# Kernel tuning notes

Hardware: AMD Instinct MI355X
Metric: run time of the kernel (lower is better)

The kernel has to match this reference:

```python
import jax, jax.numpy as jnp
import numpy as np

B, N, DIM = 4, 2048, 128
K = 32            # num_nearest_neighbors
FF = 4            # fourier_features
M_DIM = 16
EDGE_IN = FF * 2 + DIM * 2 + 1  # 265


def setup_inputs() -> dict:
    key = jax.random.key(0)
    ks = jax.random.split(key, 16)
    std = 0.001  # init_eps normal init for Linear weights
    p = {
        "feats": jax.random.normal(ks[0], (B, N, DIM), jnp.float32),
        "coors": jax.random.normal(ks[1], (B, N, 3), jnp.float32),
        # edge_mlp: Linear(265, 530) -> SiLU -> Linear(530, 16) -> SiLU
        "eW1": jax.random.normal(ks[2], (EDGE_IN, EDGE_IN * 2), jnp.float32) * std,
        "eb1": jax.random.normal(ks[3], (EDGE_IN * 2,), jnp.float32) * std,
        "eW2": jax.random.normal(ks[4], (EDGE_IN * 2, M_DIM), jnp.float32) * std,
        "eb2": jax.random.normal(ks[5], (M_DIM,), jnp.float32) * std,
        # coors_mlp: Linear(16, 64) -> SiLU -> Linear(64, 1)
        "cW1": jax.random.normal(ks[6], (M_DIM, M_DIM * 4), jnp.float32) * std,
        "cb1": jax.random.normal(ks[7], (M_DIM * 4,), jnp.float32) * std,
        "cW2": jax.random.normal(ks[8], (M_DIM * 4, 1), jnp.float32) * std,
        "cb2": jax.random.normal(ks[9], (1,), jnp.float32) * std,
        # node_mlp: Linear(144, 256) -> SiLU -> Linear(256, 128)
        "nW1": jax.random.normal(ks[10], (DIM + M_DIM, DIM * 2), jnp.float32) * std,
        "nb1": jax.random.normal(ks[11], (DIM * 2,), jnp.float32) * std,
        "nW2": jax.random.normal(ks[12], (DIM * 2, DIM), jnp.float32) * std,
        "nb2": jax.random.normal(ks[13], (DIM,), jnp.float32) * std,
    }
    return p


def _egnn_fwd(feats, coors, eW1, eb1, eW2, eb2, cW1, cb1, cW2, cb2, nW1, nb1, nW2, nb2):
    # all-pairs squared distances: [b, n, n]
    rel_coors_full = coors[:, :, None, :] - coors[:, None, :, :]
    rel_dist = jnp.sum(rel_coors_full * rel_coors_full, axis=-1)

    # top-k nearest (smallest distance) -> indices [b, n, k]
    _, idx = jax.lax.top_k(-rel_dist, K)

    # gather neighbor coords / feats per batch: [b, n, k, *]
    coors_j = jax.vmap(lambda x, i: x[i])(coors, idx)
    feats_j = jax.vmap(lambda x, i: x[i])(feats, idx)
    rel_coors = coors[:, :, None, :] - coors_j                     # b n k 3
    d = jnp.take_along_axis(rel_dist, idx, axis=2)[..., None]       # b n k 1

    # fourier encode distances: [b, n, k, 2*FF + 1]
    scales = 2.0 ** jnp.arange(FF, dtype=feats.dtype)               # [FF]
    xs = d[..., None] / scales                                      # b n k 1 FF
    enc = jnp.concatenate([jnp.sin(xs), jnp.cos(xs), d[..., None]], axis=-1)
    enc = enc[..., 0, :]                                            # b n k (2FF+1)

    feats_i = jnp.broadcast_to(feats[:, :, None, :], feats_j.shape)
    edge_input = jnp.concatenate([feats_i, feats_j, enc], axis=-1)  # b n k 265

    # edge MLP -> messages m_ij [b, n, k, m_dim]
    h = jax.nn.silu(edge_input @ eW1 + eb1)
    m_ij = jax.nn.silu(h @ eW2 + eb2)

    # coors MLP -> per-edge coordinate weights [b, n, k]
    cw = (jax.nn.silu(m_ij @ cW1 + cb1) @ cW2 + cb2)[..., 0]
    coors_out = jnp.einsum('bij,bijc->bic', cw, rel_coors) + coors

    # node update: sum-pool messages, concat with feats, MLP + residual
    m_i = jnp.sum(m_ij, axis=-2)                                    # b n m_dim
    node_in = jnp.concatenate([feats, m_i], axis=-1)
    node_out = jax.nn.silu(node_in @ nW1 + nb1) @ nW2 + nb2 + feats
    return node_out, coors_out


def reference(feats, coors, eW1, eb1, eW2, eb2, cW1, cb1, cW2, cb2, nW1, nb1, nW2, nb2):
    return _egnn_fwd(feats, coors, eW1, eb1, eW2, eb2, cW1, cb1, cW2, cb2, nW1, nb1, nW2, nb2)
```

## Files before the change

kernel.cpp:

```cpp
#include <hip/hip_runtime.h>
#include <hip/hip_bf16.h>
#include <math.h>

#define Bb 4
#define Nn 2048
#define DIMd 128
#define Kk 32
#define H1 530
#define PW2 530
#define MD 16
#define NDH 256
#define NDI 144
#define TOPK_BLKS (Bb*Nn/4)
#define PMAT_BLKS (Bb*Nn/32)

typedef float f32x2 __attribute__((ext_vector_type(2)));
typedef float f32x4 __attribute__((ext_vector_type(4)));
typedef short s16x8 __attribute__((ext_vector_type(8)));

__device__ __forceinline__ unsigned short f2bf(float f){
    union { float f; unsigned u; } v; v.f = f;
    unsigned r = v.u + 0x7FFFu + ((v.u >> 16) & 1u);
    return (unsigned short)(r >> 16);
}
__device__ __forceinline__ float silu_f(float x){
    float e = __builtin_amdgcn_exp2f(x * -1.442695041f);
    return x * __builtin_amdgcn_rcpf(1.0f + e);
}
__device__ __forceinline__ f32x2 silu2(f32x2 x){
    float e0 = __builtin_amdgcn_exp2f(x[0] * -1.442695041f);
    float e1 = __builtin_amdgcn_exp2f(x[1] * -1.442695041f);
    f32x2 r;
    r[0] = x[0] * __builtin_amdgcn_rcpf(1.0f + e0);
    r[1] = x[1] * __builtin_amdgcn_rcpf(1.0f + e1);
    return r;
}
__device__ __forceinline__ unsigned cvt_pk_bf16(float a, float b){
    unsigned r;
    asm("v_cvt_pk_bf16_f32 %0, %1, %2" : "=v"(r) : "v"(a), "v"(b));
    return r;
}

__global__ __launch_bounds__(256) void fragw_kernel(const float* __restrict__ eW1,
        const float* __restrict__ eW2,
        unsigned short* __restrict__ W1F, unsigned short* __restrict__ WPF,
        unsigned short* __restrict__ W2F2){
    int i0 = blockIdx.x * 256 + threadIdx.x;
    int stride = gridDim.x * 256;
    for (int i = i0; i < 34*5*512; i += stride){
        int j = i & 7, lane = (i >> 3) & 63, t = i >> 9;
        int ks = t % 5, nt = t / 5;
        int cg = nt*16 + (lane & 15);
        int k = ks*32 + ((lane >> 4) << 3) + j;
        float v = 0.f;
        if (cg < H1){
            if (k < 128) v = eW1[(size_t)(128+k)*H1 + cg];
            else if (k < 137) v = eW1[(size_t)(256+(k-128))*H1 + cg];
        }
        W1F[i] = f2bf(v);
    }
    for (int i = i0; i < 34*4*512; i += stride){
        int j = i & 7, lane = (i >> 3) & 63, t = i >> 9;
        int ks = t & 3, nt = t >> 2;
        int cg = nt*16 + (lane & 15);
        int k = ks*32 + ((lane >> 4) << 3) + j;
        float v = (cg < H1) ? eW1[(size_t)k*H1 + cg] : 0.f;
        WPF[i] = f2bf(v);
    }
    for (int i = i0; i < 34*512; i += stride){
        int j = i & 7, lane = (i >> 3) & 63, nt = i >> 9;
        int kl = ((lane >> 4) << 3) + j;
        int col = lane & 15;
        int row = nt*16 + kl;
        float v = (kl < 16 && row < H1) ? eW2[(size_t)row*MD + col] : 0.f;
        W2F2[i] = f2bf(v);
    }
}

__global__ __launch_bounds__(256) void prep_kernel(const float* __restrict__ coors,
        const float* __restrict__ feats,
        const unsigned short* __restrict__ WPF, const float* __restrict__ eb1,
        int* __restrict__ idx_ws, float* __restrict__ dv_ws, float* __restrict__ P){
    int bid = blockIdx.x;
    int tid = threadIdx.x;
    if (bid < TOPK_BLKS){
        int w = tid >> 6, lane = tid & 63;
        int node = bid * 4 + w;
        int b = node >> 11;
        const float* cbp = coors + (size_t)b * Nn * 3;
        float cx = coors[node*3+0], cy = coors[node*3+1], cz = coors[node*3+2];
        float d[32];
        #pragma unroll
        for (int t = 0; t < 32; t++){
            int j = t*64 + lane;
            float dx = cx - cbp[j*3+0], dy = cy - cbp[j*3+1], dz = cz - cbp[j*3+2];
            d[t] = dx*dx + dy*dy + dz*dz;
        }
        float md = d[0]; int mj = lane;
        #pragma unroll
        for (int t = 1; t < 32; t++){
            int jt = t*64 + lane;
            if (d[t] < md){ md = d[t]; mj = jt; }
        }
        for (int r = 0; r < Kk; r++){
            float bd = md; int bj = mj;
            #pragma unroll
            for (int off = 32; off; off >>= 1){
                float d2 = __shfl_xor(bd, off); int j2 = __shfl_xor(bj, off);
                if (d2 < bd || (d2 == bd && j2 < bj)){ bd = d2; bj = j2; }
            }
            if (lane == 0){
                idx_ws[node*Kk + r] = bj;
                dv_ws[node*Kk + r] = bd;
            }
            if (mj == bj){
                md = 3.4e38f; mj = 0x7fffffff;
                #pragma unroll
                for (int t = 0; t < 32; t++){
                    int jt = t*64 + lane;
                    if (jt == bj) d[t] = 3.4e38f;
                    if (d[t] < md){ md = d[t]; mj = jt; }
                }
            }
        }
    } else {
        int wid = tid >> 6, lane = tid & 63;
        int node0 = (bid - TOPK_BLKS) * 32;
        int kg = (lane >> 4) * 8;
        s16x8 af[2][4];
        #pragma unroll
        for (int m = 0; m < 2; m++){
            const float* fr = feats + (size_t)(node0 + m*16 + (lane & 15)) * DIMd;
            #pragma unroll
            for (int ks = 0; ks < 4; ks++){
                f32x4 lo = *(const f32x4*)(fr + ks*32 + kg);
                f32x4 hi = *(const f32x4*)(fr + ks*32 + kg + 4);
                union { s16x8 v; unsigned u[4]; } pk;
                pk.u[0] = cvt_pk_bf16(lo[0], lo[1]); pk.u[1] = cvt_pk_bf16(lo[2], lo[3]);
                pk.u[2] = cvt_pk_bf16(hi[0], hi[1]); pk.u[3] = cvt_pk_bf16(hi[2], hi[3]);
                af[m][ks] = pk.v;
            }
        }
        const s16x8* WPFv = (const s16x8*)WPF;
        for (int nt = wid; nt < 34; nt += 4){
            f32x4 acc0 = {0,0,0,0}, acc1 = {0,0,0,0};
            #pragma unroll
            for (int ks = 0; ks < 4; ks++){
                s16x8 bb = WPFv[(nt*4 + ks)*64 + lane];
                acc0 = __builtin_amdgcn_mfma_f32_16x16x32_bf16(af[0][ks], bb, acc0, 0, 0, 0);
                acc1 = __builtin_amdgcn_mfma_f32_16x16x32_bf16(af[1][ks], bb, acc1, 0, 0, 0);
            }
            int cg = nt*16 + (lane & 15);
            if (cg < H1){
                float b = eb1[cg];
                int r0 = (lane >> 4) * 4;
                #pragma unroll
                for (int r = 0; r < 4; r++){
                    P[(size_t)(node0 + r0 + r)*PW2 + cg]      = acc0[r] + b;
                    P[(size_t)(node0 + 16 + r0 + r)*PW2 + cg] = acc1[r] + b;
                }
            }
        }
    }
}

__global__ __launch_bounds__(256, 6) void edge_kernel(
        const float* __restrict__ feats, const float* __restrict__ eb2,
        const float* __restrict__ P, const unsigned short* __restrict__ W1F,
        const unsigned short* __restrict__ W2F2,
        const int* __restrict__ idx_ws, const float* __restrict__ dv_ws,
        float* __restrict__ m_ws){
    __shared__ float Pi_lds[544];
    __shared__ __align__(16) unsigned short aenc[Kk][32];
    __shared__ int js[Kk];
    __shared__ float m_red[4][Kk][MD+1];

    int node = blockIdx.x; int tid = threadIdx.x;
    int b = node >> 11;
    int wid = tid >> 6, lane = tid & 63;

    const float* Pn = P + (size_t)node*PW2;
    Pi_lds[tid]       = Pn[tid];
    { int c = tid + 256; Pi_lds[c] = (c < PW2) ? Pn[c] : 0.f; }
    if (tid < 32){ int c = 512 + tid; Pi_lds[c] = (c < PW2) ? Pn[c] : 0.f; }
    if (tid < Kk){
        int j = idx_ws[node*Kk + tid];
        float dv = dv_ws[node*Kk + tid];
        js[tid] = j;
        unsigned short e[9];
        e[0] = f2bf(sinf(dv));        e[1] = f2bf(sinf(dv*0.5f));
        e[2] = f2bf(sinf(dv*0.25f));  e[3] = f2bf(sinf(dv*0.125f));
        e[4] = f2bf(cosf(dv));        e[5] = f2bf(cosf(dv*0.5f));
        e[6] = f2bf(cosf(dv*0.25f));  e[7] = f2bf(cosf(dv*0.125f));
        e[8] = f2bf(dv);
        #pragma unroll
        for (int q = 0; q < 9; q++) aenc[tid][q] = e[q];
        #pragma unroll
        for (int q = 9; q < 32; q++) aenc[tid][q] = 0;
    }
    __syncthreads();

    int kg = (lane >> 4) * 8;
    int grp = lane >> 4, n16 = lane & 15;
    s16x8 af[2][5];
    #pragma unroll
    for (int m = 0; m < 2; m++){
        int row = m*16 + n16;
        int jgl = (b << 11) + js[row];
        const float* fr = feats + (size_t)jgl * DIMd;
        #pragma unroll
        for (int ks = 0; ks < 4; ks++){
            f32x4 lo = *(const f32x4*)(fr + ks*32 + kg);
            f32x4 hi = *(const f32x4*)(fr + ks*32 + kg + 4);
            union { s16x8 v; unsigned u[4]; } pk;
            pk.u[0] = cvt_pk_bf16(lo[0], lo[1]); pk.u[1] = cvt_pk_bf16(lo[2], lo[3]);
            pk.u[2] = cvt_pk_bf16(hi[0], hi[1]); pk.u[3] = cvt_pk_bf16(hi[2], hi[3]);
            af[m][ks] = pk.v;
        }
        af[m][4] = *(const s16x8*)(&aenc[row][kg]);
    }

    int addr1 = ((((2*grp)    ) << 4) | n16) << 2;
    int addr2 = ((((2*grp) + 1) << 4) | n16) << 2;

    const s16x8* W1Fv  = (const s16x8*)W1F;
    const s16x8* W2F2v = (const s16x8*)W2F2;
    f32x4 macc0 = {0,0,0,0}, macc1 = {0,0,0,0};
    for (int nt = wid; nt < 34; nt += 4){
        f32x4 acc0 = {0,0,0,0}, acc1 = {0,0,0,0};
        #pragma unroll
        for (int ks = 0; ks < 5; ks++){
            s16x8 aw = W1Fv[(nt*5 + ks)*64 + lane];
            acc0 = __builtin_amdgcn_mfma_f32_16x16x32_bf16(aw, af[0][ks], acc0, 0, 0, 0);
            acc1 = __builtin_amdgcn_mfma_f32_16x16x32_bf16(aw, af[1][ks], acc1, 0, 0, 0);
        }
        s16x8 w2a = W2F2v[nt*64 + lane];
        int cgb = nt*16 + grp*4;
        float x0[4], x1[4];
        #pragma unroll
        for (int r = 0; r < 4; r++){
            float pic = Pi_lds[cgb + r];
            x0[r] = silu_f(acc0[r] + pic);
            x1[r] = silu_f(acc1[r] + pic);
        }
        unsigned p00 = cvt_pk_bf16(x0[0], x0[1]), p01 = cvt_pk_bf16(x0[2], x0[3]);
        unsigned p10 = cvt_pk_bf16(x1[0], x1[1]), p11 = cvt_pk_bf16(x1[2], x1[3]);
        union { s16x8 v; int u[4]; } b0, b1;
        b0.u[0] = __builtin_amdgcn_ds_bpermute(addr1, (int)p00);
        b0.u[1] = __builtin_amdgcn_ds_bpermute(addr1, (int)p01);
        b0.u[2] = __builtin_amdgcn_ds_bpermute(addr2, (int)p00);
        b0.u[3] = __builtin_amdgcn_ds_bpermute(addr2, (int)p01);
        b1.u[0] = __builtin_amdgcn_ds_bpermute(addr1, (int)p10);
        b1.u[1] = __builtin_amdgcn_ds_bpermute(addr1, (int)p11);
        b1.u[2] = __builtin_amdgcn_ds_bpermute(addr2, (int)p10);
        b1.u[3] = __builtin_amdgcn_ds_bpermute(addr2, (int)p11);
        macc0 = __builtin_amdgcn_mfma_f32_16x16x32_bf16(w2a, b0.v, macc0, 0, 0, 0);
        macc1 = __builtin_amdgcn_mfma_f32_16x16x32_bf16(w2a, b1.v, macc1, 0, 0, 0);
    }
    #pragma unroll
    for (int r = 0; r < 4; r++){
        m_red[wid][n16][grp*4 + r]      = macc0[r];
        m_red[wid][16 + n16][grp*4 + r] = macc1[r];
    }
    __syncthreads();
    #pragma unroll
    for (int t = tid; t < Kk*MD; t += 256){
        int n = t >> 4, f = t & 15;
        float s = m_red[0][n][f] + m_red[1][n][f] + m_red[2][n][f] + m_red[3][n][f];
        m_ws[(size_t)node*(Kk*MD) + t] = silu_f(s + eb2[f]);
    }
}

__global__ __launch_bounds__(256) void finish_kernel(const float* __restrict__ feats,
        const float* __restrict__ coors,
        const float* __restrict__ m_ws, const int* __restrict__ idx_ws,
        const float* __restrict__ cW1, const float* __restrict__ cb1,
        const float* __restrict__ cW2, const float* __restrict__ cb2,
        const float* __restrict__ nW1, const float* __restrict__ nb1,
        const float* __restrict__ nW2, const float* __restrict__ nb2,
        float* __restrict__ out, float* __restrict__ coors_out){
    __shared__ float msh[8][Kk][MD+1];
    __shared__ float insT[NDI][12];
    __shared__ float hsdT[NDH][12];
    int tid = threadIdx.x;
    int node0 = blockIdx.x * 8;
    const float* mp = m_ws + (size_t)node0*(Kk*MD);
    for (int t = tid; t < 8*Kk*MD; t += 256)
        msh[t >> 9][(t >> 4) & 31][t & 15] = mp[t];
    for (int t = tid; t < 8*DIMd; t += 256)
        insT[t & 127][t >> 7] = feats[(size_t)node0*DIMd + t];
    int nl = tid >> 5, n = tid & 31;
    int node = node0 + nl;
    int b = node >> 11;
    int j = idx_ws[node*Kk + n];
    int jg = (b << 11) + j;
    float rx = coors[node*3+0] - coors[jg*3+0];
    float ry = coors[node*3+1] - coors[jg*3+1];
    float rz = coors[node*3+2] - coors[jg*3+2];
    __syncthreads();
    if (tid < 128){
        int m = tid >> 4, f = tid & 15;
        float s = 0.f;
        #pragma unroll
        for (int q = 0; q < Kk; q++) s += msh[m][q][f];
        insT[DIMd + f][m] = s;
    }
    float mv[MD];
    #pragma unroll
    for (int f = 0; f < MD; f++) mv[f] = msh[nl][n][f];
    float p = 0.f;
    #pragma unroll 4
    for (int ug = 0; ug < 16; ug++){
        f32x4 a4 = *(const f32x4*)(cb1 + ug*4);
        #pragma unroll
        for (int f = 0; f < MD; f++){
            f32x4 w4 = *(const f32x4*)(cW1 + f*64 + ug*4);
            a4 += (f32x4){mv[f],mv[f],mv[f],mv[f]} * w4;
        }
        f32x4 c4 = *(const f32x4*)(cW2 + ug*4);
        p += silu_f(a4[0])*c4[0] + silu_f(a4[1])*c4[1]
           + silu_f(a4[2])*c4[2] + silu_f(a4[3])*c4[3];
    }
    float cw = p + cb2[0];
    float vx = cw*rx, vy = cw*ry, vz = cw*rz;
    #pragma unroll
    for (int off = 1; off < 32; off <<= 1){
        vx += __shfl_xor(vx, off); vy += __shfl_xor(vy, off); vz += __shfl_xor(vz, off);
    }
    if (n == 0){
        coors_out[node*3+0] = vx + coors[node*3+0];
        coors_out[node*3+1] = vy + coors[node*3+1];
        coors_out[node*3+2] = vz + coors[node*3+2];
    }
    __syncthreads();
    float bias = nb1[tid];
    f32x2 acc[4];
    #pragma unroll
    for (int q = 0; q < 4; q++) acc[q] = (f32x2){bias, bias};
    for (int k = 0; k < NDI; k++){
        float wv = nW1[(size_t)k*NDH + tid];
        f32x2 w2 = {wv, wv};
        acc[0] += *(const f32x2*)&insT[k][0] * w2;
        acc[1] += *(const f32x2*)&insT[k][2] * w2;
        acc[2] += *(const f32x2*)&insT[k][4] * w2;
        acc[3] += *(const f32x2*)&insT[k][6] * w2;
    }
    #pragma unroll
    for (int q = 0; q < 4; q++) *(f32x2*)&hsdT[tid][2*q] = silu2(acc[q]);
    __syncthreads();
    int c = tid & 127, half = tid >> 7;
    float b2 = nb2[c];
    f32x2 a0 = {b2, b2}, a1 = {b2, b2};
    for (int k = 0; k < NDH; k++){
        float wv = nW2[(size_t)k*DIMd + c];
        f32x2 w2 = {wv, wv};
        a0 += *(const f32x2*)&hsdT[k][half*4]     * w2;
        a1 += *(const f32x2*)&hsdT[k][half*4 + 2] * w2;
    }
    #pragma unroll
    for (int q = 0; q < 4; q++){
        int m = half*4 + q;
        float v = (q < 2) ? a0[q & 1] : a1[q & 1];
        out[(size_t)(node0+m)*DIMd + c] = v + feats[(size_t)(node0+m)*DIMd + c];
    }
}

extern "C" void kernel_launch(void* const* d_in, const int* in_sizes, int n_in,
                              void* d_out, int out_size, void* d_ws, size_t ws_size,
                              hipStream_t stream){
    const float* feats = (const float*)d_in[0];
    const float* coors = (const float*)d_in[1];
    const float* eW1 = (const float*)d_in[2];
    const float* eb1 = (const float*)d_in[3];
    const float* eW2 = (const float*)d_in[4];
    const float* eb2 = (const float*)d_in[5];
    const float* cW1 = (const float*)d_in[6];
    const float* cb1 = (const float*)d_in[7];
    const float* cW2 = (const float*)d_in[8];
    const float* cb2 = (const float*)d_in[9];
    const float* nW1 = (const float*)d_in[10];
    const float* nb1 = (const float*)d_in[11];
    const float* nW2 = (const float*)d_in[12];
    const float* nb2 = (const float*)d_in[13];
    float* out = (float*)d_out;
    float* coors_out = out + (size_t)Bb*Nn*DIMd;

    char* ws = (char*)d_ws;
    size_t off = 0;
    int*   idx_ws = (int*)(ws + off);   off += (1u<<20);
    float* dv_ws  = (float*)(ws + off); off += (1u<<20);
    float* Pd     = (float*)(ws + off); off += 17367040u;
    float* m_ws   = (float*)(ws + off); off += 16777216u;
    unsigned short* W1F  = (unsigned short*)(ws + off); off += 174080u;
    unsigned short* WPF  = (unsigned short*)(ws + off); off += 139264u;
    unsigned short* W2F2 = (unsigned short*)(ws + off); off += 34816u;

    fragw_kernel<<<256, 256, 0, stream>>>(eW1, eW2, W1F, WPF, W2F2);
    prep_kernel<<<TOPK_BLKS + PMAT_BLKS, 256, 0, stream>>>(coors, feats, WPF, eb1,
                                                           idx_ws, dv_ws, Pd);
    edge_kernel<<<Bb*Nn, 256, 0, stream>>>(feats, eb2, Pd, W1F, W2F2,
                                           idx_ws, dv_ws, m_ws);
    finish_kernel<<<Bb*Nn/8, 256, 0, stream>>>(feats, coors, m_ws, idx_ws,
                                               cW1, cb1, cW2, cb2,
                                               nW1, nb1, nW2, nb2, out, coors_out);
}
```

Baseline: 297.3 us.

## Process two nodes per edge-kernel block to reuse W1 fragment loads

Each edge_kernel block now handles two nodes (64 edges) instead of one. Each W1/W2 weight fragment loaded from global memory feeds four MFMA column tiles instead of two, halving weight traffic per edge. The bpermute lane mapping is also changed. In exchange the kernel holds twice as many A fragments and accumulators in registers, so the launch bound drops from 6 to 4 blocks per SIMD. The grid is also halved, which could reduce latency hiding.

```diff
diff --git a/kernel.cpp b/kernel.cpp
--- a/kernel.cpp
+++ b/kernel.cpp
@@ -164,49 +164,53 @@
     }
 }
 
-__global__ __launch_bounds__(256, 6) void edge_kernel(
+__global__ __launch_bounds__(256, 4) void edge_kernel(
         const float* __restrict__ feats, const float* __restrict__ eb2,
         const float* __restrict__ P, const unsigned short* __restrict__ W1F,
         const unsigned short* __restrict__ W2F2,
         const int* __restrict__ idx_ws, const float* __restrict__ dv_ws,
         float* __restrict__ m_ws){
-    __shared__ float Pi_lds[544];
-    __shared__ __align__(16) unsigned short aenc[Kk][32];
-    __shared__ int js[Kk];
-    __shared__ float m_red[4][Kk][MD+1];
-
-    int node = blockIdx.x; int tid = threadIdx.x;
-    int b = node >> 11;
+    __shared__ float Pi_lds[2][544];
+    __shared__ __align__(16) unsigned short aenc[2][Kk][32];
+    __shared__ int js[2][Kk];
+    __shared__ float m_red[4][2][Kk][MD+1];
+
+    int node0 = blockIdx.x * 2;
+    int tid = threadIdx.x;
+    int b = node0 >> 11;
     int wid = tid >> 6, lane = tid & 63;
 
-    const float* Pn = P + (size_t)node*PW2;
-    Pi_lds[tid]       = Pn[tid];
-    { int c = tid + 256; Pi_lds[c] = (c < PW2) ? Pn[c] : 0.f; }
-    if (tid < 32){ int c = 512 + tid; Pi_lds[c] = (c < PW2) ? Pn[c] : 0.f; }
-    if (tid < Kk){
-        int j = idx_ws[node*Kk + tid];
-        float dv = dv_ws[node*Kk + tid];
-        js[tid] = j;
-        unsigned short e[9];
-        e[0] = f2bf(sinf(dv));        e[1] = f2bf(sinf(dv*0.5f));
-        e[2] = f2bf(sinf(dv*0.25f));  e[3] = f2bf(sinf(dv*0.125f));
-        e[4] = f2bf(cosf(dv));        e[5] = f2bf(cosf(dv*0.5f));
-        e[6] = f2bf(cosf(dv*0.25f));  e[7] = f2bf(cosf(dv*0.125f));
-        e[8] = f2bf(dv);
-        #pragma unroll
-        for (int q = 0; q < 9; q++) aenc[tid][q] = e[q];
-        #pragma unroll
-        for (int q = 9; q < 32; q++) aenc[tid][q] = 0;
+    for (int c = tid; c < 2*544; c += 256){
+        int nn = (c >= 544) ? 1 : 0;
+        int cc = c - nn*544;
+        Pi_lds[nn][cc] = (cc < PW2) ? P[(size_t)(node0+nn)*PW2 + cc] : 0.f;
+    }
+    if (tid < 64){
+        int nn = tid >> 5, e = tid & 31;
+        int j = idx_ws[(node0+nn)*Kk + e];
+        float dv = dv_ws[(node0+nn)*Kk + e];
+        js[nn][e] = j;
+        unsigned short ev[9];
+        ev[0] = f2bf(sinf(dv));        ev[1] = f2bf(sinf(dv*0.5f));
+        ev[2] = f2bf(sinf(dv*0.25f));  ev[3] = f2bf(sinf(dv*0.125f));
+        ev[4] = f2bf(cosf(dv));        ev[5] = f2bf(cosf(dv*0.5f));
+        ev[6] = f2bf(cosf(dv*0.25f));  ev[7] = f2bf(cosf(dv*0.125f));
+        ev[8] = f2bf(dv);
+        #pragma unroll
+        for (int q = 0; q < 9; q++) aenc[nn][e][q] = ev[q];
+        #pragma unroll
+        for (int q = 9; q < 32; q++) aenc[nn][e][q] = 0;
     }
     __syncthreads();
 
     int kg = (lane >> 4) * 8;
     int grp = lane >> 4, n16 = lane & 15;
-    s16x8 af[2][5];
-    #pragma unroll
-    for (int m = 0; m < 2; m++){
+    s16x8 af[4][5];
+    #pragma unroll
+    for (int s = 0; s < 4; s++){
+        int nn = s >> 1, m = s & 1;
         int row = m*16 + n16;
-        int jgl = (b << 11) + js[row];
+        int jgl = (b << 11) + js[nn][row];
         const float* fr = feats + (size_t)jgl * DIMd;
         #pragma unroll
         for (int ks = 0; ks < 4; ks++){
@@ -215,59 +219,94 @@
             union { s16x8 v; unsigned u[4]; } pk;
             pk.u[0] = cvt_pk_bf16(lo[0], lo[1]); pk.u[1] = cvt_pk_bf16(lo[2], lo[3]);
             pk.u[2] = cvt_pk_bf16(hi[0], hi[1]); pk.u[3] = cvt_pk_bf16(hi[2], hi[3]);
-            af[m][ks] = pk.v;
-        }
-        af[m][4] = *(const s16x8*)(&aenc[row][kg]);
-    }
-
-    int addr1 = ((((2*grp)    ) << 4) | n16) << 2;
-    int addr2 = ((((2*grp) + 1) << 4) | n16) << 2;
+            af[s][ks] = pk.v;
+        }
+        af[s][4] = *(const s16x8*)(&aenc[nn][row][kg]);
+    }
+
+    int s1 = ((grp & 1) << 1) | (grp >> 1);
+    int s2 = s1 ^ 1;
+    int addr1 = ((s1 << 4) | n16) << 2;
+    int addr2 = ((s2 << 4) | n16) << 2;
 
     const s16x8* W1Fv  = (const s16x8*)W1F;
     const s16x8* W2F2v = (const s16x8*)W2F2;
-    f32x4 macc0 = {0,0,0,0}, macc1 = {0,0,0,0};
+    f32x4 macc0 = {0,0,0,0}, macc1 = {0,0,0,0}, macc2 = {0,0,0,0}, macc3 = {0,0,0,0};
     for (int nt = wid; nt < 34; nt += 4){
-        f32x4 acc0 = {0,0,0,0}, acc1 = {0,0,0,0};
+        f32x4 acc0 = {0,0,0,0}, acc1 = {0,0,0,0}, acc2 = {0,0,0,0}, acc3 = {0,0,0,0};
         #pragma unroll
         for (int ks = 0; ks < 5; ks++){
             s16x8 aw = W1Fv[(nt*5 + ks)*64 + lane];
             acc0 = __builtin_amdgcn_mfma_f32_16x16x32_bf16(aw, af[0][ks], acc0, 0, 0, 0);
             acc1 = __builtin_amdgcn_mfma_f32_16x16x32_bf16(aw, af[1][ks], acc1, 0, 0, 0);
+            acc2 = __builtin_amdgcn_mfma_f32_16x16x32_bf16(aw, af[2][ks], acc2, 0, 0, 0);
+            acc3 = __builtin_amdgcn_mfma_f32_16x16x32_bf16(aw, af[3][ks], acc3, 0, 0, 0);
         }
         s16x8 w2a = W2F2v[nt*64 + lane];
         int cgb = nt*16 + grp*4;
-        float x0[4], x1[4];
-        #pragma unroll
-        for (int r = 0; r < 4; r++){
-            float pic = Pi_lds[cgb + r];
-            x0[r] = silu_f(acc0[r] + pic);
-            x1[r] = silu_f(acc1[r] + pic);
-        }
-        unsigned p00 = cvt_pk_bf16(x0[0], x0[1]), p01 = cvt_pk_bf16(x0[2], x0[3]);
-        unsigned p10 = cvt_pk_bf16(x1[0], x1[1]), p11 = cvt_pk_bf16(x1[2], x1[3]);
-        union { s16x8 v; int u[4]; } b0, b1;
-        b0.u[0] = __builtin_amdgcn_ds_bpermute(addr1, (int)p00);
-        b0.u[1] = __builtin_amdgcn_ds_bpermute(addr1, (int)p01);
-        b0.u[2] = __builtin_amdgcn_ds_bpermute(addr2, (int)p00);
-        b0.u[3] = __builtin_amdgcn_ds_bpermute(addr2, (int)p01);
-        b1.u[0] = __builtin_amdgcn_ds_bpermute(addr1, (int)p10);
-        b1.u[1] = __builtin_amdgcn_ds_bpermute(addr1, (int)p11);
-        b1.u[2] = __builtin_amdgcn_ds_bpermute(addr2, (int)p10);
-        b1.u[3] = __builtin_amdgcn_ds_bpermute(addr2, (int)p11);
-        macc0 = __builtin_amdgcn_mfma_f32_16x16x32_bf16(w2a, b0.v, macc0, 0, 0, 0);
-        macc1 = __builtin_amdgcn_mfma_f32_16x16x32_bf16(w2a, b1.v, macc1, 0, 0, 0);
+        {
+            float x[4];
+            #pragma unroll
+            for (int r = 0; r < 4; r++) x[r] = silu_f(acc0[r] + Pi_lds[0][cgb + r]);
+            unsigned p0 = cvt_pk_bf16(x[0], x[1]), p1 = cvt_pk_bf16(x[2], x[3]);
+            union { s16x8 v; int u[4]; } bb;
+            bb.u[0] = __builtin_amdgcn_ds_bpermute(addr1, (int)p0);
+            bb.u[1] = __builtin_amdgcn_ds_bpermute(addr1, (int)p1);
+            bb.u[2] = __builtin_amdgcn_ds_bpermute(addr2, (int)p0);
+            bb.u[3] = __builtin_amdgcn_ds_bpermute(addr2, (int)p1);
+            macc0 = __builtin_amdgcn_mfma_f32_16x16x32_bf16(w2a, bb.v, macc0, 0, 0, 0);
+        }
+        {
+            float x[4];
+            #pragma unroll
+            for (int r = 0; r < 4; r++) x[r] = silu_f(acc1[r] + Pi_lds[0][cgb + r]);
+            unsigned p0 = cvt_pk_bf16(x[0], x[1]), p1 = cvt_pk_bf16(x[2], x[3]);
+            union { s16x8 v; int u[4]; } bb;
+            bb.u[0] = __builtin_amdgcn_ds_bpermute(addr1, (int)p0);
+            bb.u[1] = __builtin_amdgcn_ds_bpermute(addr1, (int)p1);
+            bb.u[2] = __builtin_amdgcn_ds_bpermute(addr2, (int)p0);
+            bb.u[3] = __builtin_amdgcn_ds_bpermute(addr2, (int)p1);
+            macc1 = __builtin_amdgcn_mfma_f32_16x16x32_bf16(w2a, bb.v, macc1, 0, 0, 0);
+        }
+        {
+            float x[4];
+            #pragma unroll
+            for (int r = 0; r < 4; r++) x[r] = silu_f(acc2[r] + Pi_lds[1][cgb + r]);
+            unsigned p0 = cvt_pk_bf16(x[0], x[1]), p1 = cvt_pk_bf16(x[2], x[3]);
+            union { s16x8 v; int u[4]; } bb;
+            bb.u[0] = __builtin_amdgcn_ds_bpermute(addr1, (int)p0);
+            bb.u[1] = __builtin_amdgcn_ds_bpermute(addr1, (int)p1);
+            bb.u[2] = __builtin_amdgcn_ds_bpermute(addr2, (int)p0);
+            bb.u[3] = __builtin_amdgcn_ds_bpermute(addr2, (int)p1);
+            macc2 = __builtin_amdgcn_mfma_f32_16x16x32_bf16(w2a, bb.v, macc2, 0, 0, 0);
+        }
+        {
+            float x[4];
+            #pragma unroll
+            for (int r = 0; r < 4; r++) x[r] = silu_f(acc3[r] + Pi_lds[1][cgb + r]);
+            unsigned p0 = cvt_pk_bf16(x[0], x[1]), p1 = cvt_pk_bf16(x[2], x[3]);
+            union { s16x8 v; int u[4]; } bb;
+            bb.u[0] = __builtin_amdgcn_ds_bpermute(addr1, (int)p0);
+            bb.u[1] = __builtin_amdgcn_ds_bpermute(addr1, (int)p1);
+            bb.u[2] = __builtin_amdgcn_ds_bpermute(addr2, (int)p0);
+            bb.u[3] = __builtin_amdgcn_ds_bpermute(addr2, (int)p1);
+            macc3 = __builtin_amdgcn_mfma_f32_16x16x32_bf16(w2a, bb.v, macc3, 0, 0, 0);
+        }
     }
     #pragma unroll
     for (int r = 0; r < 4; r++){
-        m_red[wid][n16][grp*4 + r]      = macc0[r];
-        m_red[wid][16 + n16][grp*4 + r] = macc1[r];
+        m_red[wid][0][n16][grp*4 + r]      = macc0[r];
+        m_red[wid][0][16 + n16][grp*4 + r] = macc1[r];
+        m_red[wid][1][n16][grp*4 + r]      = macc2[r];
+        m_red[wid][1][16 + n16][grp*4 + r] = macc3[r];
     }
     __syncthreads();
-    #pragma unroll
-    for (int t = tid; t < Kk*MD; t += 256){
-        int n = t >> 4, f = t & 15;
-        float s = m_red[0][n][f] + m_red[1][n][f] + m_red[2][n][f] + m_red[3][n][f];
-        m_ws[(size_t)node*(Kk*MD) + t] = silu_f(s + eb2[f]);
+    for (int t = tid; t < 2*Kk*MD; t += 256){
+        int nn = t >> 9, rem = t & 511;
+        int n = rem >> 4, f = rem & 15;
+        float s = m_red[0][nn][n][f] + m_red[1][nn][n][f]
+                + m_red[2][nn][n][f] + m_red[3][nn][n][f];
+        m_ws[(size_t)(node0+nn)*(Kk*MD) + rem] = silu_f(s + eb2[f]);
     }
 }
 
@@ -398,8 +437,8 @@
     fragw_kernel<<<256, 256, 0, stream>>>(eW1, eW2, W1F, WPF, W2F2);
     prep_kernel<<<TOPK_BLKS + PMAT_BLKS, 256, 0, stream>>>(coors, feats, WPF, eb1,
                                                            idx_ws, dv_ws, Pd);
-    edge_kernel<<<Bb*Nn, 256, 0, stream>>>(feats, eb2, Pd, W1F, W2F2,
-                                           idx_ws, dv_ws, m_ws);
+    edge_kernel<<<Bb*Nn/2, 256, 0, stream>>>(feats, eb2, Pd, W1F, W2F2,
+                                             idx_ws, dv_ws, m_ws);
     finish_kernel<<<Bb*Nn/8, 256, 0, stream>>>(feats, coors, m_ws, idx_ws,
                                                cW1, cb1, cW2, cb2,
                                                nW1, nb1, nW2, nb2, out, coors_out);
```

Measured after the change: 326.3 us. 9.7% more time.
